# Kernel tuning notes

Measured on AMD Instinct MI355X. Metric: run time of the kernel, lower is better.

The kernel has to match this reference:

```python
import jax, jax.numpy as jnp
import numpy as np
from math import sqrt

B, H, S, D = 4, 16, 2048, 64
NEG = -1000000000.0

def setup_inputs() -> dict:
    key = jax.random.key(0)
    kq, kk, kv, km = jax.random.split(key, 4)
    Q = jax.random.normal(kq, (B, H, S, D), dtype=jnp.float32)
    K = jax.random.normal(kk, (B, H, S, D), dtype=jnp.float32)
    V = jax.random.normal(kv, (B, H, S, D), dtype=jnp.float32)
    mask = jax.random.uniform(km, (B, 1, S, S)) < 0.1
    return {"Q": Q, "K": K, "V": V, "mask": mask}

def reference(Q, K, V, mask) -> jnp.ndarray:
    # scores: [B,H,S,S]
    scores = jnp.einsum('bhqd,bhkd->bhqk', Q, K)
    scores = jnp.where(mask, NEG, scores)
    attn = jax.nn.softmax(scores / sqrt(Q.shape[-1]), axis=-1)
    return jnp.einsum('bhqk,bhkd->bhqd', attn, V)
```

## Files before the change

### kernel.cpp

```cpp
#include <hip/hip_runtime.h>


#define SEQ 2048
#define DIM 64
#define NBH 64
#define LOG2E 1.44269504088896340736f
#define SCL (0.125f * LOG2E)
#define NEG_SCALED -1.25e8f

typedef short bf16x8 __attribute__((ext_vector_type(8)));
typedef float f32x4 __attribute__((ext_vector_type(4)));
typedef float f32x16 __attribute__((ext_vector_type(16)));

static __device__ __forceinline__ unsigned short f2bf(float f) {
    unsigned int u = __float_as_uint(f);
    u += 0x7fffu + ((u >> 16) & 1u);
    return (unsigned short)(u >> 16);
}

#define GLD16(gp, lp) __builtin_amdgcn_global_load_lds( \
    (const __attribute__((address_space(1))) unsigned int*)(gp), \
    (__attribute__((address_space(3))) unsigned int*)(lp), 16, 0, 0)

__global__ __launch_bounds__(256)
void prep_all_kernel(const float* __restrict__ K, const float* __restrict__ V,
                     const int* __restrict__ M,
                     unsigned short* __restrict__ Fb, unsigned int* __restrict__ Mpt) {
    const int x = blockIdx.x;
    const int t = threadIdx.x;
    if (x < 1024) {
        __shared__ unsigned int Wt[64][8];
        const int m  = x;
        const int b  = m >> 8;
        const int q0 = ((m >> 3) & 31) * 64;
        const int k0 = (m & 7) * 256;
        const int w  = t >> 6, l = t & 63;
        #pragma unroll 4
        for (int row = 0; row < 16; ++row) {
            const int q = q0 + w * 16 + row;
            int4 v4 = *(const int4*)(M + ((size_t)b * SEQ + q) * SEQ + k0 + l * 4);
            unsigned int nib = (unsigned int)(v4.x != 0) | ((unsigned int)(v4.y != 0) << 1)
                             | ((unsigned int)(v4.z != 0) << 2) | ((unsigned int)(v4.w != 0) << 3);
            unsigned int v = nib << (4 * (l & 7));
            v |= __shfl_xor(v, 1);
            v |= __shfl_xor(v, 2);
            v |= __shfl_xor(v, 4);
            if ((l & 7) == 0) Wt[w * 16 + row][l >> 3] = v;
        }
        __syncthreads();
        {
            const int q = t & 63, g0 = t >> 6;
            #pragma unroll
            for (int gg = 0; gg < 2; ++gg) {
                const int g = g0 + gg * 4;
                const int G = (k0 >> 5) + g;
                Mpt[(((size_t)b * 32 + (G >> 1)) * SEQ + q0 + q) * 2 + (G & 1)] = Wt[q][g];
            }
        }
    } else if (x < 3072) {
        const int kb = x - 1024;
        const int bh = kb >> 5;
        const int g  = kb & 31;
        const float* Kg = K + ((size_t)bh * SEQ + g * 64) * DIM;
        unsigned short* Fo = Fb + (((size_t)bh * 32 + g) * 8192);
        #pragma unroll
        for (int i = 0; i < 2; ++i) {
            const int u   = i * 256 + t;
            const int sub = u >> 8;
            const int dc  = (u >> 6) & 3;
            const int ln  = u & 63;
            const int hh  = ln >> 5;
            const int q32 = ln & 31;
            const float* kp = Kg + (size_t)(sub * 32 + q32) * DIM + dc * 16 + hh * 8;
            float4 a = *(const float4*)kp;
            float4 b2 = *(const float4*)(kp + 4);
            union { uint4 q4; unsigned short s[8]; } w;
            w.s[0] = f2bf(a.x); w.s[1] = f2bf(a.y); w.s[2] = f2bf(a.z); w.s[3] = f2bf(a.w);
            w.s[4] = f2bf(b2.x); w.s[5] = f2bf(b2.y); w.s[6] = f2bf(b2.z); w.s[7] = f2bf(b2.w);
            *(uint4*)(Fo + (size_t)u * 8) = w.q4;
        }
    } else {
        __shared__ __align__(16) unsigned short T[64 * 64];
        const int vb = x - 3072;
        const int bh = vb >> 5;
        const int g  = vb & 31;
        const int k0 = g * 64;
        {
            const float* Vb = V + ((size_t)bh * SEQ + k0) * DIM;
            #pragma unroll
            for (int j = 0; j < 4; ++j) {
                const int fi = (j * 256 + t) * 4;
                const int kk = fi >> 6;
                const int d0 = fi & 63;
                float4 f = *(const float4*)(Vb + fi);
                const int u  = (kk & ~12) | ((kk & 4) << 1) | ((kk & 8) >> 1);
                const int cs = (d0 >> 4) ^ ((u >> 3) & 3);
                union { uint2 q; unsigned short s[4]; } w4;
                w4.s[0] = f2bf(f.x); w4.s[1] = f2bf(f.y);
                w4.s[2] = f2bf(f.z); w4.s[3] = f2bf(f.w);
                *(uint2*)&T[u * 64 + cs * 16 + (d0 & 15)] = w4.q;
            }
        }
        __syncthreads();
        {
            const int p   = t & 31;
            const int w2  = t >> 5;
            const int sub = w2 >> 2;
            const int kk  = (w2 >> 1) & 1;
            const int hh  = w2 & 1;
            const int dh  = p >> 4;
            const int q32a = (2 * p) & 31;
            const int ub  = sub * 32 + kk * 16 + hh * 8;
            const unsigned int* T32 = (const unsigned int*)T;
            union { uint4 q4; unsigned short s[8]; } o0, o1;
            #pragma unroll
            for (int j = 0; j < 8; ++j) {
                const int u  = ub + j;
                const int ch = (p >> 3) ^ ((u >> 3) & 3);
                unsigned int v = T32[u * 32 + ch * 8 + (p & 7)];
                o0.s[j] = (unsigned short)v;
                o1.s[j] = (unsigned short)(v >> 16);
            }
            unsigned short* dst = Fb + (((size_t)bh * 32 + g) * 8192) + 4096
                                + sub * 2048 + kk * 1024 + dh * 512 + hh * 256 + q32a * 8;
            *(uint4*)dst       = o0.q4;
            *(uint4*)(dst + 8) = o1.q4;
        }
    }
}


#define TILE_QK(sc, sub, mqv)                                                   \
    {                                                                           \
        _Pragma("unroll")                                                       \
        for (int r = 0; r < 16; ++r) {                                          \
            const int s_ = (r & 3) + 8 * (r >> 2);                              \
            sc[r] = __int_as_float(__builtin_amdgcn_sbfe(mqv, s_, 1) & 0xC2C80000u); \
        }                                                                       \
        __builtin_amdgcn_s_setprio(1);                                          \
        _Pragma("unroll")                                                       \
        for (int dc = 0; dc < 4; ++dc) {                                        \
            bf16x8 kf = *(const bf16x8*)(Bl + (sub) * 2048 + dc * 512);         \
            sc = __builtin_amdgcn_mfma_f32_32x32x16_bf16(kf, qf[dc], sc, 0, 0, 0); \
        }                                                                       \
        __builtin_amdgcn_s_setprio(0);                                          \
    }

#define TILE_SMPV(sc, sub)                                                      \
    {                                                                           \
        float pv_[16];                                                          \
        _Pragma("unroll")                                                       \
        for (int r = 0; r < 16; ++r) pv_[r] = __builtin_amdgcn_exp2f(sc[r]);    \
        _Pragma("unroll")                                                       \
        for (int r = 0; r < 16; r += 4) {                                       \
            ls0 += pv_[r + 0]; ls1 += pv_[r + 1];                               \
            ls2 += pv_[r + 2]; ls3 += pv_[r + 3];                               \
        }                                                                       \
        unsigned int pk_[8];                                                    \
        _Pragma("unroll")                                                       \
        for (int m = 0; m < 8; ++m)                                             \
            asm("v_cvt_pk_bf16_f32 %0, %1, %2"                                  \
                : "=v"(pk_[m]) : "v"(pv_[2 * m]), "v"(pv_[2 * m + 1]));         \
        __builtin_amdgcn_s_setprio(1);                                          \
        _Pragma("unroll")                                                       \
        for (int kk = 0; kk < 2; ++kk) {                                        \
            union { unsigned int u[4]; bf16x8 v; } fr;                          \
            fr.u[0] = pk_[4 * kk + 0]; fr.u[1] = pk_[4 * kk + 1];               \
            fr.u[2] = pk_[4 * kk + 2]; fr.u[3] = pk_[4 * kk + 3];               \
            _Pragma("unroll")                                                   \
            for (int dh = 0; dh < 2; ++dh) {                                    \
                bf16x8 vf = *(const bf16x8*)(Bl + 4096 + (sub) * 2048 + kk * 1024 + dh * 512); \
                acc[dh] = __builtin_amdgcn_mfma_f32_32x32x16_bf16(vf, fr.v, acc[dh], 0, 0, 0); \
            }                                                                   \
        }                                                                       \
        __builtin_amdgcn_s_setprio(0);                                          \
    }

__global__ __launch_bounds__(256, 4)
void attn_main_kernel(const float* __restrict__ Q,
                      const unsigned short* __restrict__ Fb,
                      const unsigned int* __restrict__ Mpt,
                      float* __restrict__ O)
{
    const int n    = blockIdx.y * gridDim.x + blockIdx.x;
    const int bh   = ((n & 7) << 3) | (n >> 7);
    const int q0   = ((n >> 3) & 15) * 128;
    const int b    = bh >> 4;
    const int tid  = threadIdx.x;
    const int wave = tid >> 6;
    const int lane = tid & 63;
    const int h    = lane >> 5;
    const int q32  = lane & 31;
    const int sh4  = 4 * h;

    __shared__ __align__(16) unsigned short Blob[2][8192];

    const unsigned short* Fbh = Fb + (size_t)bh * 32 * 8192;

    bf16x8 qf[4];
    {
        const float* qp = Q + ((size_t)bh * SEQ + q0 + wave * 32 + q32) * DIM + h * 8;
        #pragma unroll
        for (int dc = 0; dc < 4; ++dc) {
            float4 xx = *(const float4*)(qp + dc * 16);
            float4 yy = *(const float4*)(qp + dc * 16 + 4);
            qf[dc][0] = (short)f2bf(xx.x * SCL); qf[dc][1] = (short)f2bf(xx.y * SCL);
            qf[dc][2] = (short)f2bf(xx.z * SCL); qf[dc][3] = (short)f2bf(xx.w * SCL);
            qf[dc][4] = (short)f2bf(yy.x * SCL); qf[dc][5] = (short)f2bf(yy.y * SCL);
            qf[dc][6] = (short)f2bf(yy.z * SCL); qf[dc][7] = (short)f2bf(yy.w * SCL);
        }
    }

    const unsigned short* fg = Fbh + wave * 2048 + lane * 8;

    const unsigned int* mp = Mpt + ((size_t)b * 32 * SEQ + q0 + wave * 32 + q32) * 2;

    f32x16 acc[2];
    #pragma unroll
    for (int i = 0; i < 16; ++i) { acc[0][i] = 0.f; acc[1][i] = 0.f; }
    float ls0 = 0.f, ls1 = 0.f, ls2 = 0.f, ls3 = 0.f;

    #pragma unroll
    for (int c = 0; c < 4; ++c)
        GLD16(fg + c * 512, &Blob[0][wave * 2048 + c * 512]);
    uint2 mwp = *(const uint2*)mp;

    #pragma unroll 2
    for (int g = 0; g < SEQ / 64; ++g) {
        __syncthreads();

        uint2 mwpn = {0u, 0u};
        if (g + 1 < SEQ / 64) {
            const unsigned short* fgn = fg + (size_t)(g + 1) * 8192;
            const int nb = (g + 1) & 1;
            #pragma unroll
            for (int c = 0; c < 4; ++c)
                GLD16(fgn + c * 512, &Blob[nb][wave * 2048 + c * 512]);
            mwpn = *(const uint2*)(mp + (size_t)(g + 1) * 2 * SEQ);
        }

        const unsigned short* Bl = &Blob[g & 1][0] + lane * 8;
        const unsigned int mq0 = mwp.x >> sh4;
        const unsigned int mq1 = mwp.y >> sh4;

        f32x16 sc0, sc1;
        TILE_QK(sc0, 0, mq0);
        TILE_QK(sc1, 1, mq1);
        TILE_SMPV(sc0, 0);
        TILE_SMPV(sc1, 1);

        mwp = mwpn;
    }

    float lsum = (ls0 + ls1) + (ls2 + ls3);
    lsum += __shfl_xor(lsum, 32);
    const float inv = 1.f / lsum;
    float* orow = O + ((size_t)bh * SEQ + q0 + wave * 32 + q32) * DIM;
    #pragma unroll
    for (int dh = 0; dh < 2; ++dh) {
        #pragma unroll
        for (int r23 = 0; r23 < 4; ++r23) {
            float4 w;
            w.x = acc[dh][4 * r23 + 0] * inv;
            w.y = acc[dh][4 * r23 + 1] * inv;
            w.z = acc[dh][4 * r23 + 2] * inv;
            w.w = acc[dh][4 * r23 + 3] * inv;
            *(float4*)(orow + dh * 32 + r23 * 8 + h * 4) = w;
        }
    }
}

__global__ __launch_bounds__(256)
void attn_fallback_kernel(const float* __restrict__ Q,
                          const float* __restrict__ K,
                          const float* __restrict__ V,
                          const int* __restrict__ mask,
                          float* __restrict__ O)
{
    const int bh   = blockIdx.y;
    const int b    = bh >> 4;
    const int q0   = blockIdx.x * 64;
    const int tid  = threadIdx.x;
    const int wave = tid >> 6;
    const int lane = tid & 63;
    const int quad = lane >> 4;
    const int l16  = lane & 15;

    __shared__ __align__(16) unsigned short Klds[32][72];
    __shared__ __align__(16) unsigned short VT[64][40];
    __shared__ __align__(16) unsigned short Plds[4][16][40];

    const float* Qb = Q + (size_t)bh * SEQ * DIM;
    const float* Kb = K + (size_t)bh * SEQ * DIM;
    const float* Vb = V + (size_t)bh * SEQ * DIM;
    const int*   Mb = mask + (size_t)b * SEQ * SEQ;

    const int qrow_frag = q0 + wave * 16 + l16;
    bf16x8 qf0, qf1;
    {
        const float* qp = Qb + (size_t)qrow_frag * DIM + quad * 8;
        #pragma unroll
        for (int i = 0; i < 8; ++i) {
            qf0[i] = (short)f2bf(qp[i]);
            qf1[i] = (short)f2bf(qp[32 + i]);
        }
    }

    f32x4 acc[4];
    #pragma unroll
    for (int dg = 0; dg < 4; ++dg) acc[dg] = (f32x4){0.f, 0.f, 0.f, 0.f};
    float mrowv[4] = {-INFINITY, -INFINITY, -INFINITY, -INFINITY};
    float lrow[4] = {0.f, 0.f, 0.f, 0.f};

    const int skey = tid >> 3;
    const int sd0  = (tid & 7) * 8;
    const int vkey = tid & 31;
    const int vd0  = (tid >> 5) * 8;
    const int qrow_m = q0 + wave * 16 + quad * 4;

    for (int kb = 0; kb < SEQ; kb += 32) {
        __syncthreads();
        {
            const float* kp = Kb + (size_t)(kb + skey) * DIM + sd0;
            union { uint4 u4; unsigned short s[8]; } kw;
            #pragma unroll
            for (int i = 0; i < 8; ++i) kw.s[i] = f2bf(kp[i]);
            *(uint4*)&Klds[skey][sd0] = kw.u4;
        }
        {
            const float* vp = Vb + (size_t)(kb + vkey) * DIM + vd0;
            #pragma unroll
            for (int i = 0; i < 8; ++i) VT[vd0 + i][vkey] = f2bf(vp[i]);
        }
        __syncthreads();

        f32x4 scr[2];
        scr[0] = (f32x4){0.f, 0.f, 0.f, 0.f};
        scr[1] = (f32x4){0.f, 0.f, 0.f, 0.f};
        #pragma unroll
        for (int nt = 0; nt < 2; ++nt) {
            bf16x8 kf0 = *(const bf16x8*)&Klds[nt * 16 + l16][quad * 8];
            bf16x8 kf1 = *(const bf16x8*)&Klds[nt * 16 + l16][32 + quad * 8];
            scr[nt] = __builtin_amdgcn_mfma_f32_16x16x32_bf16(qf0, kf0, scr[nt], 0, 0, 0);
            scr[nt] = __builtin_amdgcn_mfma_f32_16x16x32_bf16(qf1, kf1, scr[nt], 0, 0, 0);
        }

        float x[2][4];
        #pragma unroll
        for (int nt = 0; nt < 2; ++nt)
            #pragma unroll
            for (int r = 0; r < 4; ++r) {
                int mv = Mb[(size_t)(qrow_m + r) * SEQ + kb + nt * 16 + l16];
                x[nt][r] = mv ? NEG_SCALED : scr[nt][r] * 0.125f;
            }

        float p[2][4];
        #pragma unroll
        for (int r = 0; r < 4; ++r) {
            float rm = fmaxf(x[0][r], x[1][r]);
            #pragma unroll
            for (int off = 1; off < 16; off <<= 1)
                rm = fmaxf(rm, __shfl_xor(rm, off, 16));
            float mn = fmaxf(mrowv[r], rm);
            float alpha = exp2f((mrowv[r] - mn) * LOG2E);
            mrowv[r] = mn;
            float p0 = exp2f((x[0][r] - mn) * LOG2E);
            float p1 = exp2f((x[1][r] - mn) * LOG2E);
            p[0][r] = p0; p[1][r] = p1;
            float rs = p0 + p1;
            #pragma unroll
            for (int off = 1; off < 16; off <<= 1)
                rs += __shfl_xor(rs, off, 16);
            lrow[r] = lrow[r] * alpha + rs;
            #pragma unroll
            for (int dg = 0; dg < 4; ++dg)
                acc[dg][r] *= alpha;
        }

        #pragma unroll
        for (int nt = 0; nt < 2; ++nt)
            #pragma unroll
            for (int r = 0; r < 4; ++r)
                Plds[wave][quad * 4 + r][nt * 16 + l16] = f2bf(p[nt][r]);

        bf16x8 pf = *(const bf16x8*)&Plds[wave][l16][quad * 8];

        #pragma unroll
        for (int dg = 0; dg < 4; ++dg) {
            bf16x8 vf = *(const bf16x8*)&VT[dg * 16 + l16][quad * 8];
            acc[dg] = __builtin_amdgcn_mfma_f32_16x16x32_bf16(pf, vf, acc[dg], 0, 0, 0);
        }
    }

    float* Ob = O + (size_t)bh * SEQ * DIM;
    #pragma unroll
    for (int r = 0; r < 4; ++r) {
        float inv = 1.f / lrow[r];
        #pragma unroll
        for (int dg = 0; dg < 4; ++dg)
            Ob[(size_t)(qrow_m + r) * DIM + dg * 16 + l16] = acc[dg][r] * inv;
    }
}

extern "C" void kernel_launch(void* const* d_in, const int* in_sizes, int n_in,
                              void* d_out, int out_size, void* d_ws, size_t ws_size,
                              hipStream_t stream) {
    const float* Q = (const float*)d_in[0];
    const float* K = (const float*)d_in[1];
    const float* V = (const float*)d_in[2];
    const int* mask = (const int*)d_in[3];
    float*        O = (float*)d_out;

    const size_t szF = (size_t)NBH * 32 * 8192 * 2;
    const size_t szM = (size_t)4 * SEQ * (SEQ / 32) * 4;
    const size_t need = szF + szM;

    if (ws_size >= need) {
        unsigned short* Fb = (unsigned short*)d_ws;
        unsigned int*  Mpt = (unsigned int*)((char*)d_ws + szF);

        prep_all_kernel<<<dim3(5120), 256, 0, stream>>>(K, V, mask, Fb, Mpt);
        attn_main_kernel<<<dim3(SEQ / 128, NBH), 256, 0, stream>>>(Q, Fb, Mpt, O);
    } else {
        attn_fallback_kernel<<<dim3(SEQ / 64, NBH), 256, 0, stream>>>(Q, K, V, mask, O);
    }
}
```

Baseline: 267.3 us.

## Load K/V fragments directly from global into registers, drop LDS staging

Replaces the LDS double-buffered global_load_lds staging of K/V fragments with direct per-wave global loads into registers, software-pipelined one 32-key subtile ahead. Blocks shrink to 2 waves (64 query rows), the grid becomes 1D with 2048 blocks, and the mask-word layout is changed to one word per 32-key group. This removes the per-iteration __syncthreads and LDS traffic, at the cost of each wave re-fetching K/V from L2 with no sharing across waves and higher register pressure.

After: 283.4 us. +6.0%, slower.

```diff
diff --git a/kernel.cpp b/kernel.cpp
--- a/kernel.cpp
+++ b/kernel.cpp
@@ -17,10 +17,6 @@
     u += 0x7fffu + ((u >> 16) & 1u);
     return (unsigned short)(u >> 16);
 }
-
-#define GLD16(gp, lp) __builtin_amdgcn_global_load_lds( \
-    (const __attribute__((address_space(1))) unsigned int*)(gp), \
-    (__attribute__((address_space(3))) unsigned int*)(lp), 16, 0, 0)
 
 __global__ __launch_bounds__(256)
 void prep_all_kernel(const float* __restrict__ K, const float* __restrict__ V,
@@ -53,8 +49,7 @@
             #pragma unroll
             for (int gg = 0; gg < 2; ++gg) {
                 const int g = g0 + gg * 4;
-                const int G = (k0 >> 5) + g;
-                Mpt[(((size_t)b * 32 + (G >> 1)) * SEQ + q0 + q) * 2 + (G & 1)] = Wt[q][g];
+                Mpt[((size_t)b * 64 + (k0 >> 5) + g) * SEQ + q0 + q] = Wt[q][g];
             }
         }
     } else if (x < 3072) {
@@ -130,23 +125,28 @@
 }
 
 
-#define TILE_QK(sc, sub, mqv)                                                   \
+#define LDFRAG(fr4, bp)                                                         \
+    { fr4[0] = *(const bf16x8*)(bp);                                            \
+      fr4[1] = *(const bf16x8*)((bp) + 512);                                    \
+      fr4[2] = *(const bf16x8*)((bp) + 1024);                                   \
+      fr4[3] = *(const bf16x8*)((bp) + 1536); }
+
+#define TILE_QK_R(sc, kf, mwv)                                                  \
     {                                                                           \
+        const unsigned int mq_ = (mwv) >> sh4;                                  \
         _Pragma("unroll")                                                       \
         for (int r = 0; r < 16; ++r) {                                          \
             const int s_ = (r & 3) + 8 * (r >> 2);                              \
-            sc[r] = __int_as_float(__builtin_amdgcn_sbfe(mqv, s_, 1) & 0xC2C80000u); \
+            sc[r] = __int_as_float(__builtin_amdgcn_sbfe(mq_, s_, 1) & 0xC2C80000u); \
         }                                                                       \
         __builtin_amdgcn_s_setprio(1);                                          \
         _Pragma("unroll")                                                       \
-        for (int dc = 0; dc < 4; ++dc) {                                        \
-            bf16x8 kf = *(const bf16x8*)(Bl + (sub) * 2048 + dc * 512);         \
-            sc = __builtin_amdgcn_mfma_f32_32x32x16_bf16(kf, qf[dc], sc, 0, 0, 0); \
-        }                                                                       \
+        for (int dc = 0; dc < 4; ++dc)                                          \
+            sc = __builtin_amdgcn_mfma_f32_32x32x16_bf16(kf[dc], qf[dc], sc, 0, 0, 0); \
         __builtin_amdgcn_s_setprio(0);                                          \
     }
 
-#define TILE_SMPV(sc, sub)                                                      \
+#define TILE_SMPV_R(sc, vf)                                                     \
     {                                                                           \
         float pv_[16];                                                          \
         _Pragma("unroll")                                                       \
@@ -167,24 +167,22 @@
             union { unsigned int u[4]; bf16x8 v; } fr;                          \
             fr.u[0] = pk_[4 * kk + 0]; fr.u[1] = pk_[4 * kk + 1];               \
             fr.u[2] = pk_[4 * kk + 2]; fr.u[3] = pk_[4 * kk + 3];               \
-            _Pragma("unroll")                                                   \
-            for (int dh = 0; dh < 2; ++dh) {                                    \
-                bf16x8 vf = *(const bf16x8*)(Bl + 4096 + (sub) * 2048 + kk * 1024 + dh * 512); \
-                acc[dh] = __builtin_amdgcn_mfma_f32_32x32x16_bf16(vf, fr.v, acc[dh], 0, 0, 0); \
-            }                                                                   \
+            acc[0] = __builtin_amdgcn_mfma_f32_32x32x16_bf16(vf[kk * 2 + 0], fr.v, acc[0], 0, 0, 0); \
+            acc[1] = __builtin_amdgcn_mfma_f32_32x32x16_bf16(vf[kk * 2 + 1], fr.v, acc[1], 0, 0, 0); \
         }                                                                       \
         __builtin_amdgcn_s_setprio(0);                                          \
     }
 
-__global__ __launch_bounds__(256, 4)
+__global__ __launch_bounds__(128, 3)
 void attn_main_kernel(const float* __restrict__ Q,
                       const unsigned short* __restrict__ Fb,
                       const unsigned int* __restrict__ Mpt,
                       float* __restrict__ O)
 {
-    const int n    = blockIdx.y * gridDim.x + blockIdx.x;
-    const int bh   = ((n & 7) << 3) | (n >> 7);
-    const int q0   = ((n >> 3) & 15) * 128;
+    const int n    = blockIdx.x;
+    const int mI   = n >> 3;
+    const int bh   = (n & 7) * 8 + (mI >> 5);
+    const int qc   = mI & 31;
     const int b    = bh >> 4;
     const int tid  = threadIdx.x;
     const int wave = tid >> 6;
@@ -192,14 +190,11 @@
     const int h    = lane >> 5;
     const int q32  = lane & 31;
     const int sh4  = 4 * h;
-
-    __shared__ __align__(16) unsigned short Blob[2][8192];
-
-    const unsigned short* Fbh = Fb + (size_t)bh * 32 * 8192;
+    const int q0   = qc * 64 + wave * 32;
 
     bf16x8 qf[4];
     {
-        const float* qp = Q + ((size_t)bh * SEQ + q0 + wave * 32 + q32) * DIM + h * 8;
+        const float* qp = Q + ((size_t)bh * SEQ + q0 + q32) * DIM + h * 8;
         #pragma unroll
         for (int dc = 0; dc < 4; ++dc) {
             float4 xx = *(const float4*)(qp + dc * 16);
@@ -211,51 +206,48 @@
         }
     }
 
-    const unsigned short* fg = Fbh + wave * 2048 + lane * 8;
-
-    const unsigned int* mp = Mpt + ((size_t)b * 32 * SEQ + q0 + wave * 32 + q32) * 2;
+    const unsigned short* pG = Fb + (size_t)bh * 32 * 8192 + lane * 8;
+    const unsigned int* mr = Mpt + (size_t)b * 64 * SEQ + (q0 + q32);
 
     f32x16 acc[2];
     #pragma unroll
     for (int i = 0; i < 16; ++i) { acc[0][i] = 0.f; acc[1][i] = 0.f; }
     float ls0 = 0.f, ls1 = 0.f, ls2 = 0.f, ls3 = 0.f;
 
-    #pragma unroll
-    for (int c = 0; c < 4; ++c)
-        GLD16(fg + c * 512, &Blob[0][wave * 2048 + c * 512]);
-    uint2 mwp = *(const uint2*)mp;
-
-    #pragma unroll 2
-    for (int g = 0; g < SEQ / 64; ++g) {
-        __syncthreads();
-
-        uint2 mwpn = {0u, 0u};
-        if (g + 1 < SEQ / 64) {
-            const unsigned short* fgn = fg + (size_t)(g + 1) * 8192;
-            const int nb = (g + 1) & 1;
-            #pragma unroll
-            for (int c = 0; c < 4; ++c)
-                GLD16(fgn + c * 512, &Blob[nb][wave * 2048 + c * 512]);
-            mwpn = *(const uint2*)(mp + (size_t)(g + 1) * 2 * SEQ);
-        }
-
-        const unsigned short* Bl = &Blob[g & 1][0] + lane * 8;
-        const unsigned int mq0 = mwp.x >> sh4;
-        const unsigned int mq1 = mwp.y >> sh4;
-
-        f32x16 sc0, sc1;
-        TILE_QK(sc0, 0, mq0);
-        TILE_QK(sc1, 1, mq1);
-        TILE_SMPV(sc0, 0);
-        TILE_SMPV(sc1, 1);
-
-        mwp = mwpn;
+    bf16x8 kA[4], kB[4], vC[4];
+    unsigned int mA, mB;
+
+    LDFRAG(kA, pG);
+    mA = mr[0];
+
+    #pragma unroll 1
+    for (int t = 0; t < 64; t += 2) {
+        LDFRAG(kB, pG + 2048);
+        mB = mr[SEQ];
+        LDFRAG(vC, pG + 4096);
+        {
+            f32x16 sc;
+            TILE_QK_R(sc, kA, mA);
+            TILE_SMPV_R(sc, vC);
+        }
+        pG += 8192;
+        mr += 2 * SEQ;
+        if (t + 2 < 64) {
+            LDFRAG(kA, pG);
+            mA = mr[0];
+        }
+        LDFRAG(vC, pG - 2048);
+        {
+            f32x16 sc;
+            TILE_QK_R(sc, kB, mB);
+            TILE_SMPV_R(sc, vC);
+        }
     }
 
     float lsum = (ls0 + ls1) + (ls2 + ls3);
     lsum += __shfl_xor(lsum, 32);
     const float inv = 1.f / lsum;
-    float* orow = O + ((size_t)bh * SEQ + q0 + wave * 32 + q32) * DIM;
+    float* orow = O + ((size_t)bh * SEQ + q0 + q32) * DIM;
     #pragma unroll
     for (int dh = 0; dh < 2; ++dh) {
         #pragma unroll
@@ -420,7 +412,7 @@
         unsigned int*  Mpt = (unsigned int*)((char*)d_ws + szF);
 
         prep_all_kernel<<<dim3(5120), 256, 0, stream>>>(K, V, mask, Fb, Mpt);
-        attn_main_kernel<<<dim3(SEQ / 128, NBH), 256, 0, stream>>>(Q, Fb, Mpt, O);
+        attn_main_kernel<<<dim3(2048), 128, 0, stream>>>(Q, Fb, Mpt, O);
     } else {
         attn_fallback_kernel<<<dim3(SEQ / 64, NBH), 256, 0, stream>>>(Q, K, V, mask, O);
     }
```

## Process 64 queries per wave to double K/V reuse from shared memory

Applied to the files above, without the earlier changes.

Each wave now handles two 32-row query halves instead of one, so each K/V fragment read from LDS feeds two MFMAs. The block tile grows to 256 queries, which halves the grid to 512 blocks and halves global K/V traffic per query. The mask bit layout in the prep kernel changes to one word per 32-key group, indexed per query row. Register pressure roughly doubles for the accumulators, so launch bounds drop to 2 blocks per CU and the loop unroll is reduced to 1.

New measurement: 276.4 us. 1.03x slower.

```diff
diff --git a/kernel.cpp b/kernel.cpp
--- a/kernel.cpp
+++ b/kernel.cpp
@@ -53,8 +53,7 @@
             #pragma unroll
             for (int gg = 0; gg < 2; ++gg) {
                 const int g = g0 + gg * 4;
-                const int G = (k0 >> 5) + g;
-                Mpt[(((size_t)b * 32 + (G >> 1)) * SEQ + q0 + q) * 2 + (G & 1)] = Wt[q][g];
+                Mpt[((size_t)b * 64 + (k0 >> 5) + g) * SEQ + q0 + q] = Wt[q][g];
             }
         }
     } else if (x < 3072) {
@@ -130,61 +129,67 @@
 }
 
 
-#define TILE_QK(sc, sub, mqv)                                                   \
+#define TILE_QK2(sc, qfh, SUBOFF, mwv)                                          \
     {                                                                           \
+        const unsigned int mq_ = (mwv) >> sh4;                                  \
         _Pragma("unroll")                                                       \
         for (int r = 0; r < 16; ++r) {                                          \
             const int s_ = (r & 3) + 8 * (r >> 2);                              \
-            sc[r] = __int_as_float(__builtin_amdgcn_sbfe(mqv, s_, 1) & 0xC2C80000u); \
+            sc[r] = __int_as_float(__builtin_amdgcn_sbfe(mq_, s_, 1) & 0xC2C80000u); \
         }                                                                       \
         __builtin_amdgcn_s_setprio(1);                                          \
         _Pragma("unroll")                                                       \
         for (int dc = 0; dc < 4; ++dc) {                                        \
-            bf16x8 kf = *(const bf16x8*)(Bl + (sub) * 2048 + dc * 512);         \
-            sc = __builtin_amdgcn_mfma_f32_32x32x16_bf16(kf, qf[dc], sc, 0, 0, 0); \
+            bf16x8 kf = *(const bf16x8*)(Bl + (SUBOFF) + dc * 512);             \
+            sc = __builtin_amdgcn_mfma_f32_32x32x16_bf16(kf, qfh[dc], sc, 0, 0, 0); \
         }                                                                       \
         __builtin_amdgcn_s_setprio(0);                                          \
     }
 
-#define TILE_SMPV(sc, sub)                                                      \
+#define TILE_SM2(sc, pk, lsv)                                                   \
     {                                                                           \
         float pv_[16];                                                          \
         _Pragma("unroll")                                                       \
         for (int r = 0; r < 16; ++r) pv_[r] = __builtin_amdgcn_exp2f(sc[r]);    \
         _Pragma("unroll")                                                       \
         for (int r = 0; r < 16; r += 4) {                                       \
-            ls0 += pv_[r + 0]; ls1 += pv_[r + 1];                               \
-            ls2 += pv_[r + 2]; ls3 += pv_[r + 3];                               \
+            lsv[0] += pv_[r + 0]; lsv[1] += pv_[r + 1];                         \
+            lsv[2] += pv_[r + 2]; lsv[3] += pv_[r + 3];                         \
         }                                                                       \
-        unsigned int pk_[8];                                                    \
         _Pragma("unroll")                                                       \
         for (int m = 0; m < 8; ++m)                                             \
             asm("v_cvt_pk_bf16_f32 %0, %1, %2"                                  \
-                : "=v"(pk_[m]) : "v"(pv_[2 * m]), "v"(pv_[2 * m + 1]));         \
+                : "=v"(pk[m]) : "v"(pv_[2 * m]), "v"(pv_[2 * m + 1]));          \
+    }
+
+#define TILE_PV2(pkA, pkB, SUBOFF)                                              \
+    {                                                                           \
         __builtin_amdgcn_s_setprio(1);                                          \
         _Pragma("unroll")                                                       \
         for (int kk = 0; kk < 2; ++kk) {                                        \
-            union { unsigned int u[4]; bf16x8 v; } fr;                          \
-            fr.u[0] = pk_[4 * kk + 0]; fr.u[1] = pk_[4 * kk + 1];               \
-            fr.u[2] = pk_[4 * kk + 2]; fr.u[3] = pk_[4 * kk + 3];               \
+            union { unsigned int u[4]; bf16x8 v; } fa, fb;                      \
+            _Pragma("unroll")                                                   \
+            for (int j = 0; j < 4; ++j) { fa.u[j] = pkA[4 * kk + j]; fb.u[j] = pkB[4 * kk + j]; } \
             _Pragma("unroll")                                                   \
             for (int dh = 0; dh < 2; ++dh) {                                    \
-                bf16x8 vf = *(const bf16x8*)(Bl + 4096 + (sub) * 2048 + kk * 1024 + dh * 512); \
-                acc[dh] = __builtin_amdgcn_mfma_f32_32x32x16_bf16(vf, fr.v, acc[dh], 0, 0, 0); \
+                bf16x8 vf = *(const bf16x8*)(Bl + 4096 + (SUBOFF) + kk * 1024 + dh * 512); \
+                acc[0][dh] = __builtin_amdgcn_mfma_f32_32x32x16_bf16(vf, fa.v, acc[0][dh], 0, 0, 0); \
+                acc[1][dh] = __builtin_amdgcn_mfma_f32_32x32x16_bf16(vf, fb.v, acc[1][dh], 0, 0, 0); \
             }                                                                   \
         }                                                                       \
         __builtin_amdgcn_s_setprio(0);                                          \
     }
 
-__global__ __launch_bounds__(256, 4)
+__global__ __launch_bounds__(256, 2)
 void attn_main_kernel(const float* __restrict__ Q,
                       const unsigned short* __restrict__ Fb,
                       const unsigned int* __restrict__ Mpt,
                       float* __restrict__ O)
 {
-    const int n    = blockIdx.y * gridDim.x + blockIdx.x;
-    const int bh   = ((n & 7) << 3) | (n >> 7);
-    const int q0   = ((n >> 3) & 15) * 128;
+    const int n    = blockIdx.x;
+    const int mI   = n >> 3;
+    const int bh   = (n & 7) * 8 + (mI >> 3);
+    const int qb   = mI & 7;
     const int b    = bh >> 4;
     const int tid  = threadIdx.x;
     const int wave = tid >> 6;
@@ -192,80 +197,102 @@
     const int h    = lane >> 5;
     const int q32  = lane & 31;
     const int sh4  = 4 * h;
+    const int q0   = qb * 256 + wave * 64;
 
     __shared__ __align__(16) unsigned short Blob[2][8192];
 
-    const unsigned short* Fbh = Fb + (size_t)bh * 32 * 8192;
-
-    bf16x8 qf[4];
-    {
-        const float* qp = Q + ((size_t)bh * SEQ + q0 + wave * 32 + q32) * DIM + h * 8;
+    bf16x8 qf[2][4];
+    #pragma unroll
+    for (int half = 0; half < 2; ++half) {
+        const float* qp = Q + ((size_t)bh * SEQ + q0 + half * 32 + q32) * DIM + h * 8;
         #pragma unroll
         for (int dc = 0; dc < 4; ++dc) {
             float4 xx = *(const float4*)(qp + dc * 16);
             float4 yy = *(const float4*)(qp + dc * 16 + 4);
-            qf[dc][0] = (short)f2bf(xx.x * SCL); qf[dc][1] = (short)f2bf(xx.y * SCL);
-            qf[dc][2] = (short)f2bf(xx.z * SCL); qf[dc][3] = (short)f2bf(xx.w * SCL);
-            qf[dc][4] = (short)f2bf(yy.x * SCL); qf[dc][5] = (short)f2bf(yy.y * SCL);
-            qf[dc][6] = (short)f2bf(yy.z * SCL); qf[dc][7] = (short)f2bf(yy.w * SCL);
-        }
-    }
-
-    const unsigned short* fg = Fbh + wave * 2048 + lane * 8;
-
-    const unsigned int* mp = Mpt + ((size_t)b * 32 * SEQ + q0 + wave * 32 + q32) * 2;
-
-    f32x16 acc[2];
-    #pragma unroll
-    for (int i = 0; i < 16; ++i) { acc[0][i] = 0.f; acc[1][i] = 0.f; }
-    float ls0 = 0.f, ls1 = 0.f, ls2 = 0.f, ls3 = 0.f;
+            qf[half][dc][0] = (short)f2bf(xx.x * SCL); qf[half][dc][1] = (short)f2bf(xx.y * SCL);
+            qf[half][dc][2] = (short)f2bf(xx.z * SCL); qf[half][dc][3] = (short)f2bf(xx.w * SCL);
+            qf[half][dc][4] = (short)f2bf(yy.x * SCL); qf[half][dc][5] = (short)f2bf(yy.y * SCL);
+            qf[half][dc][6] = (short)f2bf(yy.z * SCL); qf[half][dc][7] = (short)f2bf(yy.w * SCL);
+        }
+    }
+
+    const unsigned short* fg = Fb + (size_t)bh * 32 * 8192 + wave * 2048 + lane * 8;
+
+    const unsigned int* mpA = Mpt + (size_t)b * 64 * SEQ + (q0 + q32);
+    const unsigned int* mpB = mpA + 32;
+
+    f32x16 acc[2][2];
+    #pragma unroll
+    for (int i = 0; i < 16; ++i) {
+        acc[0][0][i] = 0.f; acc[0][1][i] = 0.f;
+        acc[1][0][i] = 0.f; acc[1][1][i] = 0.f;
+    }
+    float lsA[4] = {0.f, 0.f, 0.f, 0.f};
+    float lsB[4] = {0.f, 0.f, 0.f, 0.f};
 
     #pragma unroll
     for (int c = 0; c < 4; ++c)
         GLD16(fg + c * 512, &Blob[0][wave * 2048 + c * 512]);
-    uint2 mwp = *(const uint2*)mp;
-
-    #pragma unroll 2
+    unsigned int mwA0 = mpA[0],   mwA1 = mpA[SEQ];
+    unsigned int mwB0 = mpB[0],   mwB1 = mpB[SEQ];
+
+    #pragma unroll 1
     for (int g = 0; g < SEQ / 64; ++g) {
         __syncthreads();
 
-        uint2 mwpn = {0u, 0u};
+        unsigned int nA0 = 0, nA1 = 0, nB0 = 0, nB1 = 0;
         if (g + 1 < SEQ / 64) {
             const unsigned short* fgn = fg + (size_t)(g + 1) * 8192;
             const int nb = (g + 1) & 1;
             #pragma unroll
             for (int c = 0; c < 4; ++c)
                 GLD16(fgn + c * 512, &Blob[nb][wave * 2048 + c * 512]);
-            mwpn = *(const uint2*)(mp + (size_t)(g + 1) * 2 * SEQ);
+            nA0 = mpA[(2 * g + 2) * SEQ]; nA1 = mpA[(2 * g + 3) * SEQ];
+            nB0 = mpB[(2 * g + 2) * SEQ]; nB1 = mpB[(2 * g + 3) * SEQ];
         }
 
         const unsigned short* Bl = &Blob[g & 1][0] + lane * 8;
-        const unsigned int mq0 = mwp.x >> sh4;
-        const unsigned int mq1 = mwp.y >> sh4;
-
-        f32x16 sc0, sc1;
-        TILE_QK(sc0, 0, mq0);
-        TILE_QK(sc1, 1, mq1);
-        TILE_SMPV(sc0, 0);
-        TILE_SMPV(sc1, 1);
-
-        mwp = mwpn;
-    }
-
-    float lsum = (ls0 + ls1) + (ls2 + ls3);
-    lsum += __shfl_xor(lsum, 32);
-    const float inv = 1.f / lsum;
-    float* orow = O + ((size_t)bh * SEQ + q0 + wave * 32 + q32) * DIM;
-    #pragma unroll
-    for (int dh = 0; dh < 2; ++dh) {
-        #pragma unroll
-        for (int r23 = 0; r23 < 4; ++r23) {
-            float4 w;
-            w.x = acc[dh][4 * r23 + 0] * inv;
-            w.y = acc[dh][4 * r23 + 1] * inv;
-            w.z = acc[dh][4 * r23 + 2] * inv;
-            w.w = acc[dh][4 * r23 + 3] * inv;
-            *(float4*)(orow + dh * 32 + r23 * 8 + h * 4) = w;
+
+        {
+            f32x16 scA, scB;
+            TILE_QK2(scA, qf[0], 0, mwA0);
+            TILE_QK2(scB, qf[1], 0, mwB0);
+            unsigned int pkA[8], pkB[8];
+            TILE_SM2(scA, pkA, lsA);
+            TILE_SM2(scB, pkB, lsB);
+            TILE_PV2(pkA, pkB, 0);
+        }
+        {
+            f32x16 scA, scB;
+            TILE_QK2(scA, qf[0], 2048, mwA1);
+            TILE_QK2(scB, qf[1], 2048, mwB1);
+            unsigned int pkA[8], pkB[8];
+            TILE_SM2(scA, pkA, lsA);
+            TILE_SM2(scB, pkB, lsB);
+            TILE_PV2(pkA, pkB, 2048);
+        }
+
+        mwA0 = nA0; mwA1 = nA1; mwB0 = nB0; mwB1 = nB1;
+    }
+
+    #pragma unroll
+    for (int half = 0; half < 2; ++half) {
+        float lsum = half == 0 ? (lsA[0] + lsA[1]) + (lsA[2] + lsA[3])
+                               : (lsB[0] + lsB[1]) + (lsB[2] + lsB[3]);
+        lsum += __shfl_xor(lsum, 32);
+        const float inv = 1.f / lsum;
+        float* orow = O + ((size_t)bh * SEQ + q0 + half * 32 + q32) * DIM;
+        #pragma unroll
+        for (int dh = 0; dh < 2; ++dh) {
+            #pragma unroll
+            for (int r23 = 0; r23 < 4; ++r23) {
+                float4 w;
+                w.x = acc[half][dh][4 * r23 + 0] * inv;
+                w.y = acc[half][dh][4 * r23 + 1] * inv;
+                w.z = acc[half][dh][4 * r23 + 2] * inv;
+                w.w = acc[half][dh][4 * r23 + 3] * inv;
+                *(float4*)(orow + dh * 32 + r23 * 8 + h * 4) = w;
+            }
         }
     }
 }
@@ -420,7 +447,7 @@
         unsigned int*  Mpt = (unsigned int*)((char*)d_ws + szF);
 
         prep_all_kernel<<<dim3(5120), 256, 0, stream>>>(K, V, mask, Fb, Mpt);
-        attn_main_kernel<<<dim3(SEQ / 128, NBH), 256, 0, stream>>>(Q, Fb, Mpt, O);
+        attn_main_kernel<<<dim3(512), 256, 0, stream>>>(Q, Fb, Mpt, O);
     } else {
         attn_fallback_kernel<<<dim3(SEQ / 64, NBH), 256, 0, stream>>>(Q, K, V, mask, O);
     }
```
